# Performance work log

Measured on AMD Instinct MI355X. Metric: run time of the kernel, lower is better.

The kernel has to match this reference:

```python
import jax, jax.numpy as jnp
import numpy as np

N = 8192
H = 512
TAU = 0.8
LAM = 0.5
EPS = 1e-8


def setup_inputs() -> dict:
    key = jax.random.key(0)
    k1, k2, k3, k4, k5 = jax.random.split(key, 5)
    xavier_std = 1.414 * np.sqrt(2.0 / (H + H))  # xavier_normal_ with gain=1.414
    return {
        "z_mp": jax.random.normal(k1, (N, H), dtype=jnp.float32),
        "z_sc": jax.random.normal(k2, (N, H), dtype=jnp.float32),
        "pos": jax.random.randint(k3, (N, N), 0, 2, dtype=jnp.int32),
        "W1": (jax.random.normal(k4, (H, H), dtype=jnp.float32) * xavier_std),
        "b1": jnp.zeros((H,), dtype=jnp.float32),
        "W2": (jax.random.normal(k5, (H, H), dtype=jnp.float32) * xavier_std),
        "b2": jnp.zeros((H,), dtype=jnp.float32),
    }


def _proj(z, W1, b1, W2, b2):
    # nn.Linear applies x @ W.T + b
    h = jax.nn.elu(z @ W1.T + b1)
    return h @ W2.T + b2


def _sim(z1, z2, tau):
    # exp(cosine_similarity / tau), computed as in the original:
    # dot(z1, z2.T) / (|z1| |z2|.T) / tau
    n1 = jnp.linalg.norm(z1, axis=-1, keepdims=True)  # [N,1]
    n2 = jnp.linalg.norm(z2, axis=-1, keepdims=True)  # [N,1]
    dot = z1 @ z2.T                                   # [N,N]
    return jnp.exp(dot / (n1 * n2.T) / tau)


def reference(z_mp, z_sc, pos, W1, b1, W2, b2):
    pos_f = pos.astype(jnp.float32)
    zp_mp = _proj(z_mp, W1, b1, W2, b2)
    zp_sc = _proj(z_sc, W1, b1, W2, b2)

    m_mp2sc = _sim(zp_mp, zp_sc, TAU)   # [N,N]
    m_sc2mp = m_mp2sc.T                 # [N,N]

    # row-normalize, masked log-mean (mp -> sc)
    s_mp = m_mp2sc / (jnp.sum(m_mp2sc, axis=1, keepdims=True) + EPS)
    lori_mp = -jnp.mean(jnp.log(jnp.sum(s_mp * pos_f, axis=-1)))

    # row-normalize, masked log-mean (sc -> mp)
    s_sc = m_sc2mp / (jnp.sum(m_sc2mp, axis=1, keepdims=True) + EPS)
    lori_sc = -jnp.mean(jnp.log(jnp.sum(s_sc * pos_f, axis=-1)))

    return LAM * lori_mp + (1.0 - LAM) * lori_sc
```

## Files before the change

### kernel.cpp

```cpp
#include <hip/hip_runtime.h>
#include <stdint.h>


#define NN 8192
#define HH 512
#define TAUF 0.8f
#define EPSF 1e-8f
#define NW (NN / 32)

typedef __attribute__((ext_vector_type(8))) short short8;
typedef __attribute__((ext_vector_type(4))) float f32x4;
typedef __attribute__((ext_vector_type(4))) int i32x4;
typedef __attribute__((ext_vector_type(4))) unsigned short u16x4;
typedef unsigned short u16;
typedef unsigned int u32;

typedef __attribute__((address_space(1))) void GV;
typedef __attribute__((address_space(3))) void LV;

__device__ __forceinline__ void g2l16(const void* g, void* l) {
  __builtin_amdgcn_global_load_lds((const GV*)g, (LV*)l, 16, 0, 0);
}

__device__ __forceinline__ u16 f2bf(float x) {
  u32 u = __builtin_bit_cast(u32, x);
  u = (u + 0x7fffu + ((u >> 16) & 1u)) >> 16;
  return (u16)u;
}

__device__ __forceinline__ void cast8(const float* __restrict__ in, u16* __restrict__ out, int i) {
  f32x4 a = *(const f32x4*)(in + i);
  f32x4 b = *(const f32x4*)(in + i + 4);
  u16 o[8];
  o[0] = f2bf(a.x); o[1] = f2bf(a.y); o[2] = f2bf(a.z); o[3] = f2bf(a.w);
  o[4] = f2bf(b.x); o[5] = f2bf(b.y); o[6] = f2bf(b.z); o[7] = f2bf(b.w);
  i32x4 v;
  v.x = (int)(o[0] | ((u32)o[1] << 16)); v.y = (int)(o[2] | ((u32)o[3] << 16));
  v.z = (int)(o[4] | ((u32)o[5] << 16)); v.w = (int)(o[6] | ((u32)o[7] << 16));
  *(i32x4*)(out + i) = v;
}

__global__ __launch_bounds__(256)
void prep_kernel(const int* __restrict__ pos, u32* __restrict__ P,
                 const float* __restrict__ z_mp, u16* __restrict__ zbA,
                 const float* __restrict__ z_sc, u16* __restrict__ zbB,
                 const float* __restrict__ W1, u16* __restrict__ W1b,
                 const float* __restrict__ W2, u16* __restrict__ W2b) {
  int b = blockIdx.x, tid = threadIdx.x;
  if (b < 8192) {
    int gid = b * 256 + tid;
    const int* src = pos + (size_t)gid * 32;
    u32 w = 0;
#pragma unroll
    for (int c = 0; c < 8; ++c) {
      i32x4 p = *(const i32x4*)(src + c * 4);
      w |= ((u32)p.x & 1u) << (c * 4);
      w |= ((u32)p.y & 1u) << (c * 4 + 1);
      w |= ((u32)p.z & 1u) << (c * 4 + 2);
      w |= ((u32)p.w & 1u) << (c * 4 + 3);
    }
    P[gid] = w;
  } else if (b < 10240) {
    cast8(z_mp, zbA, ((b - 8192) * 256 + tid) * 8);
  } else if (b < 12288) {
    cast8(z_sc, zbB, ((b - 10240) * 256 + tid) * 8);
  } else if (b < 12416) {
    cast8(W1, W1b, ((b - 12288) * 256 + tid) * 8);
  } else {
    cast8(W2, W2b, ((b - 12416) * 256 + tid) * 8);
  }
}

template <int EPI>
__global__ __launch_bounds__(256)
void gemm_proj(const u16* __restrict__ A1, const u16* __restrict__ A2,
               const u16* __restrict__ W, const float* __restrict__ bias,
               void* __restrict__ out1, void* __restrict__ out2) {
  __shared__ __align__(16) u16 As[128 * 32];
  __shared__ __align__(16) u16 Bs[128 * 32];
  const int tid = threadIdx.x;
  const int lane = tid & 63, w = tid >> 6;
  const int lo = lane & 15, quad = lane >> 4;
  const int wy = w >> 1, wx = w & 1;
  const u16* A; char* Out; int m0;
  if (blockIdx.y < 64) { A = A1; Out = (char*)out1; m0 = blockIdx.y * 128; }
  else                 { A = A2; Out = (char*)out2; m0 = (blockIdx.y - 64) * 128; }
  const int n0 = blockIdx.x * 128;
  const int srow = w * 16 + (lane >> 2);
  const int skel = (lane & 3) * 8;
  char* AsB = (char*)As; char* BsB = (char*)Bs;
  f32x4 acc[4][4] = {};

  for (int k0 = 0; k0 < HH; k0 += 32) {
    const u16* ga = A + (size_t)(m0 + srow) * HH + k0 + skel;
    const u16* gb = W + (size_t)(n0 + srow) * HH + k0 + skel;
    g2l16(ga, AsB + w * 1024);
    g2l16(ga + (size_t)64 * HH, AsB + w * 1024 + 4096);
    g2l16(gb, BsB + w * 1024);
    g2l16(gb + (size_t)64 * HH, BsB + w * 1024 + 4096);
    asm volatile("s_waitcnt vmcnt(0)" ::: "memory");
    __syncthreads();
    short8 aF[4], bF[4];
#pragma unroll
    for (int mi = 0; mi < 4; ++mi)
      aF[mi] = *(const short8*)(AsB + (wy * 64 + mi * 16 + lo) * 64 + quad * 16);
#pragma unroll
    for (int ni = 0; ni < 4; ++ni)
      bF[ni] = *(const short8*)(BsB + (wx * 64 + ni * 16 + lo) * 64 + quad * 16);
#pragma unroll
    for (int mi = 0; mi < 4; ++mi)
#pragma unroll
      for (int ni = 0; ni < 4; ++ni)
        acc[mi][ni] = __builtin_amdgcn_mfma_f32_16x16x32_bf16(aF[mi], bF[ni], acc[mi][ni], 0, 0, 0);
    __syncthreads();
  }
#pragma unroll
  for (int mi = 0; mi < 4; ++mi) {
    int rl = wy * 64 + mi * 16 + quad * 4;
#pragma unroll
    for (int ni = 0; ni < 4; ++ni) {
      int cl = wx * 64 + ni * 16 + lo;
      float bv = bias[n0 + cl];
#pragma unroll
      for (int r = 0; r < 4; ++r) {
        float v = acc[mi][ni][r] + bv;
        size_t idx = (size_t)(m0 + rl + r) * HH + (n0 + cl);
        if (EPI == 0) {
          if (v < 0.f) v = __expf(v) - 1.f;
          ((u16*)Out)[idx] = f2bf(v);
        } else {
          ((float*)Out)[idx] = v;
        }
      }
    }
  }
}

__global__ void norm_kernel(const float* __restrict__ zpA, u16* __restrict__ znA,
                            const float* __restrict__ zpB, u16* __restrict__ znB) {
  const int row = blockIdx.x & (NN - 1);
  const bool isA = blockIdx.x < NN;
  const float* src = (isA ? zpA : zpB) + (size_t)row * HH;
  u16* dst = (isA ? znA : znB) + (size_t)row * HH;
  const float scale = isA ? (1.0f / TAUF) : 1.0f;
  const int t = threadIdx.x;
  f32x4 v = *(const f32x4*)(src + t * 4);
  float ss = v.x * v.x + v.y * v.y + v.z * v.z + v.w * v.w;
#pragma unroll
  for (int d = 1; d < 64; d <<= 1) ss += __shfl_xor(ss, d, 64);
  __shared__ float red[2];
  if ((t & 63) == 0) red[t >> 6] = ss;
  __syncthreads();
  float inv = scale * rsqrtf(red[0] + red[1]);
  u16x4 o;
  o[0] = f2bf(v.x * inv); o[1] = f2bf(v.y * inv);
  o[2] = f2bf(v.z * inv); o[3] = f2bf(v.w * inv);
  *(u16x4*)(dst + t * 4) = o;
}

__global__ __launch_bounds__(256)
void sim_kernel(const u16* __restrict__ Az, const u16* __restrict__ Bz,
                const u32* __restrict__ Pbits,
                float* __restrict__ rowpart, float* __restrict__ posrowpart,
                float* __restrict__ colpart, float* __restrict__ poscolpart) {
  __shared__ __align__(16) u16 As[128 * 64];
  __shared__ __align__(16) u16 Bs[128 * 64];
  __shared__ u32 PBi[128 * 4];
  __shared__ u32 PBj[128 * 4];
  const int tid = threadIdx.x;
  const int lane = tid & 63, w = tid >> 6;
  const int lo = lane & 15, quad = lane >> 4;
  const int wy = w >> 1, wx = w & 1;

  const int bid = blockIdx.x + (int)gridDim.x * blockIdx.y;
  const int xcd = bid & 7, s = bid >> 3;
  const int by = xcd * 8 + (s >> 6);
  const int bx = s & 63;
  const int i0 = by * 128, j0 = bx * 128;

  const int il = tid >> 1, w2 = (tid & 1) * 2;
  const u32* PiSrc = Pbits + (size_t)(i0 + il) * NW + (j0 >> 5) + w2;
  const u32* PjSrc = Pbits + (size_t)(j0 + il) * NW + (i0 >> 5) + w2;
  u32 pa0 = PiSrc[0], pa1 = PiSrc[1], pb0 = PjSrc[0], pb1 = PjSrc[1];

  const int srow = lane >> 3;
  const int skel = (lane & 7) * 8;
  char* AsB = (char*)As; char* BsB = (char*)Bs;
  f32x4 acc[4][4] = {};

  for (int k0 = 0; k0 < HH; k0 += 64) {
    const u16* ga = Az + (size_t)(i0 + w * 32 + srow) * HH + k0 + skel;
    const u16* gb = Bz + (size_t)(j0 + w * 32 + srow) * HH + k0 + skel;
#pragma unroll
    for (int t = 0; t < 4; ++t) {
      g2l16(ga + (size_t)(t * 8) * HH, AsB + w * 4096 + t * 1024);
      g2l16(gb + (size_t)(t * 8) * HH, BsB + w * 4096 + t * 1024);
    }
    asm volatile("s_waitcnt vmcnt(0)" ::: "memory");
    __syncthreads();
    short8 aF[4][2], bF[4][2];
#pragma unroll
    for (int mi = 0; mi < 4; ++mi)
#pragma unroll
      for (int ks = 0; ks < 2; ++ks)
        aF[mi][ks] = *(const short8*)(AsB + (wy * 64 + mi * 16 + lo) * 128 + ks * 64 + quad * 16);
#pragma unroll
    for (int ni = 0; ni < 4; ++ni)
#pragma unroll
      for (int ks = 0; ks < 2; ++ks)
        bF[ni][ks] = *(const short8*)(BsB + (wx * 64 + ni * 16 + lo) * 128 + ks * 64 + quad * 16);
#pragma unroll
    for (int ks = 0; ks < 2; ++ks)
#pragma unroll
      for (int mi = 0; mi < 4; ++mi)
#pragma unroll
        for (int ni = 0; ni < 4; ++ni)
          acc[mi][ni] = __builtin_amdgcn_mfma_f32_16x16x32_bf16(aF[mi][ks], bF[ni][ks], acc[mi][ni], 0, 0, 0);
    __syncthreads();
  }

  PBi[il * 4 + w2] = pa0; PBi[il * 4 + w2 + 1] = pa1;
  PBj[il * 4 + w2] = pb0; PBj[il * 4 + w2 + 1] = pb1;

#pragma unroll
  for (int mi = 0; mi < 4; ++mi)
#pragma unroll
    for (int ni = 0; ni < 4; ++ni)
#pragma unroll
      for (int r = 0; r < 4; ++r)
        acc[mi][ni][r] = __expf(acc[mi][ni][r]);

  __syncthreads();

  const int rowb = wy * 64 + quad * 4;
  const int colb = wx * 64 + lo;

#pragma unroll
  for (int mi = 0; mi < 4; ++mi) {
    int rl = rowb + mi * 16;
    float rs[4], pr[4];
#pragma unroll
    for (int r = 0; r < 4; ++r) {
      u32 W0 = PBi[(rl + r) * 4 + wx * 2];
      u32 W1 = PBi[(rl + r) * 4 + wx * 2 + 1];
      float e0 = acc[mi][0][r], e1 = acc[mi][1][r];
      float e2 = acc[mi][2][r], e3 = acc[mi][3][r];
      rs[r] = (e0 + e1) + (e2 + e3);
      pr[r] = (((W0 >> lo) & 1u) ? e0 : 0.f) + (((W0 >> (16 + lo)) & 1u) ? e1 : 0.f) +
              (((W1 >> lo) & 1u) ? e2 : 0.f) + (((W1 >> (16 + lo)) & 1u) ? e3 : 0.f);
    }
#pragma unroll
    for (int d = 1; d < 16; d <<= 1) {
#pragma unroll
      for (int r = 0; r < 4; ++r) {
        rs[r] += __shfl_xor(rs[r], d, 64);
        pr[r] += __shfl_xor(pr[r], d, 64);
      }
    }
    if (lo == 0) {
      float* rp = rowpart + (size_t)(bx * 2 + wx) * NN;
      float* pp = posrowpart + (size_t)(bx * 2 + wx) * NN;
#pragma unroll
      for (int r = 0; r < 4; ++r) {
        rp[i0 + rl + r] = rs[r];
        pp[i0 + rl + r] = pr[r];
      }
    }
  }

#pragma unroll
  for (int ni = 0; ni < 4; ++ni) {
    int cl = colb + ni * 16;
    u32 W0 = PBj[cl * 4 + wy * 2];
    u32 W1 = PBj[cl * 4 + wy * 2 + 1];
    float cs = 0.f, pc = 0.f;
#pragma unroll
    for (int mi = 0; mi < 4; ++mi) {
      u32 W = (mi < 2) ? W0 : W1;
      int sh = (mi & 1) * 16 + quad * 4;
#pragma unroll
      for (int r = 0; r < 4; ++r) {
        float e = acc[mi][ni][r];
        cs += e;
        pc += ((W >> (sh + r)) & 1u) ? e : 0.f;
      }
    }
    cs += __shfl_xor(cs, 16, 64); cs += __shfl_xor(cs, 32, 64);
    pc += __shfl_xor(pc, 16, 64); pc += __shfl_xor(pc, 32, 64);
    if (quad == 0) {
      colpart[(size_t)(by * 2 + wy) * NN + j0 + cl] = cs;
      poscolpart[(size_t)(by * 2 + wy) * NN + j0 + cl] = pc;
    }
  }
}

__global__ __launch_bounds__(256)
void reduce1_kernel(const float* __restrict__ rowpart, const float* __restrict__ posrowpart,
                    const float* __restrict__ colpart, const float* __restrict__ poscolpart,
                    float* __restrict__ red) {
  int t = threadIdx.x;
  int i = blockIdx.x * 128 + (t >> 1);
  int half = t & 1;
  float rs = 0.f, pr = 0.f, cs = 0.f, pc = 0.f;
  for (int s = half * 64; s < half * 64 + 64; ++s) {
    rs += rowpart[(size_t)s * NN + i];
    pr += posrowpart[(size_t)s * NN + i];
    cs += colpart[(size_t)s * NN + i];
    pc += poscolpart[(size_t)s * NN + i];
  }
  rs += __shfl_xor(rs, 1, 64); pr += __shfl_xor(pr, 1, 64);
  cs += __shfl_xor(cs, 1, 64); pc += __shfl_xor(pc, 1, 64);
  float term = (half == 0) ? (__logf(pr / (rs + EPSF)) + __logf(pc / (cs + EPSF))) : 0.f;
#pragma unroll
  for (int d = 2; d < 64; d <<= 1) term += __shfl_xor(term, d, 64);
  __shared__ float rsh[4];
  if ((t & 63) == 0) rsh[t >> 6] = term;
  __syncthreads();
  if (t == 0) red[blockIdx.x] = rsh[0] + rsh[1] + rsh[2] + rsh[3];
}

__global__ void reduce2_kernel(const float* __restrict__ red, float* __restrict__ out) {
  float s = red[threadIdx.x];
#pragma unroll
  for (int d = 1; d < 64; d <<= 1) s += __shfl_xor(s, d, 64);
  if (threadIdx.x == 0) out[0] = -0.5f * s / (float)NN;
}

extern "C" void kernel_launch(void* const* d_in, const int* in_sizes, int n_in,
                              void* d_out, int out_size, void* d_ws, size_t ws_size,
                              hipStream_t stream) {
  const float* z_mp = (const float*)d_in[0];
  const float* z_sc = (const float*)d_in[1];
  const int* pos = (const int*)d_in[2];
  const float* W1 = (const float*)d_in[3];
  const float* b1 = (const float*)d_in[4];
  const float* W2 = (const float*)d_in[5];
  const float* b2 = (const float*)d_in[6];
  float* out = (float*)d_out;

  char* ws = (char*)d_ws;
  u32* Pbits = (u32*)(ws);
  u16* zbA = (u16*)(ws + 8388608);
  u16* zbB = (u16*)(ws + 16777216);
  u16* W1b = (u16*)(ws + 25165824);
  u16* W2b = (u16*)(ws + 25690112);
  u16* hA  = (u16*)(ws + 26214400);
  u16* hB  = (u16*)(ws + 34603008);
  float* zpA = (float*)(ws + 42991616);
  float* zpB = (float*)(ws + 59768832);
  u16* znA = zbA;
  u16* znB = zbB;
  float* rowpart    = (float*)(ws + 26214400);
  float* posrowpart = (float*)(ws + 30408704);
  float* colpart    = (float*)(ws + 34603008);
  float* poscolpart = (float*)(ws + 38797312);
  float* red64 = (float*)(ws + 76546048);

  prep_kernel<<<12544, 256, 0, stream>>>(pos, Pbits, z_mp, zbA, z_sc, zbB, W1, W1b, W2, W2b);

  dim3 gp(4, 128);
  gemm_proj<0><<<gp, 256, 0, stream>>>(zbA, zbB, W1b, b1, hA, hB);
  gemm_proj<1><<<gp, 256, 0, stream>>>(hA, hB, W2b, b2, zpA, zpB);

  norm_kernel<<<2 * NN, 128, 0, stream>>>(zpA, znA, zpB, znB);

  dim3 gs(64, 64);
  sim_kernel<<<gs, 256, 0, stream>>>(znA, znB, Pbits, rowpart, posrowpart, colpart, poscolpart);
  reduce1_kernel<<<64, 256, 0, stream>>>(rowpart, posrowpart, colpart, poscolpart, red64);
  reduce2_kernel<<<1, 64, 0, stream>>>(red64, out);
}
```

Baseline: 584.6 us.

## Quantize normalized embeddings to FP8 and use scaled f8f6f4 MFMA in similarity GEMM

The norm kernel now writes the unit-normalized projections as FP8 E4M3 bytes instead of bf16, and the similarity kernel consumes them with the 16x16x128 scaled f8f6f4 MFMA. K-tiles grow to 128 bytes per row, and the LDS layout uses an XOR swizzle to avoid bank conflicts. The goal is to halve the operand bandwidth and raise matrix throughput in the N×N GEMM. The cost is reduced precision on the cosine dot products, which are then exponentiated, so the loss may drift.

```diff
diff --git a/kernel.cpp b/kernel.cpp
--- a/kernel.cpp
+++ b/kernel.cpp
@@ -11,9 +11,11 @@
 typedef __attribute__((ext_vector_type(8))) short short8;
 typedef __attribute__((ext_vector_type(4))) float f32x4;
 typedef __attribute__((ext_vector_type(4))) int i32x4;
+typedef __attribute__((ext_vector_type(8))) int i32x8;
 typedef __attribute__((ext_vector_type(4))) unsigned short u16x4;
 typedef unsigned short u16;
 typedef unsigned int u32;
+typedef uint8_t u8;
 
 typedef __attribute__((address_space(1))) void GV;
 typedef __attribute__((address_space(3))) void LV;
@@ -26,6 +28,22 @@
   u32 u = __builtin_bit_cast(u32, x);
   u = (u + 0x7fffu + ((u >> 16) & 1u)) >> 16;
   return (u16)u;
+}
+
+__device__ __forceinline__ u32 f2fp8(float x) {
+  u32 u = __builtin_bit_cast(u32, x);
+  u32 s = (u >> 31) << 7;
+  float a = fabsf(x);
+  if (a >= 0.015625f) {
+    u32 b = __builtin_bit_cast(u32, a);
+    b += 0x7FFFFu + ((b >> 20) & 1u);
+    u32 e = (b >> 23) - 127u + 7u;
+    u32 m = (b >> 20) & 7u;
+    return s | (e << 3) | m;
+  } else {
+    int m = (int)rintf(a * 512.0f);
+    return s | (u32)m;
+  }
 }
 
 __device__ __forceinline__ void cast8(const float* __restrict__ in, u16* __restrict__ out, int i) {
@@ -136,12 +154,12 @@
   }
 }
 
-__global__ void norm_kernel(const float* __restrict__ zpA, u16* __restrict__ znA,
-                            const float* __restrict__ zpB, u16* __restrict__ znB) {
+__global__ void norm_kernel(const float* __restrict__ zpA, u8* __restrict__ znA,
+                            const float* __restrict__ zpB, u8* __restrict__ znB) {
   const int row = blockIdx.x & (NN - 1);
   const bool isA = blockIdx.x < NN;
   const float* src = (isA ? zpA : zpB) + (size_t)row * HH;
-  u16* dst = (isA ? znA : znB) + (size_t)row * HH;
+  u8* dst = (isA ? znA : znB) + (size_t)row * HH;
   const float scale = isA ? (1.0f / TAUF) : 1.0f;
   const int t = threadIdx.x;
   f32x4 v = *(const f32x4*)(src + t * 4);
@@ -152,19 +170,18 @@
   if ((t & 63) == 0) red[t >> 6] = ss;
   __syncthreads();
   float inv = scale * rsqrtf(red[0] + red[1]);
-  u16x4 o;
-  o[0] = f2bf(v.x * inv); o[1] = f2bf(v.y * inv);
-  o[2] = f2bf(v.z * inv); o[3] = f2bf(v.w * inv);
-  *(u16x4*)(dst + t * 4) = o;
+  u32 o = f2fp8(v.x * inv) | (f2fp8(v.y * inv) << 8) |
+          (f2fp8(v.z * inv) << 16) | (f2fp8(v.w * inv) << 24);
+  *(u32*)(dst + t * 4) = o;
 }
 
 __global__ __launch_bounds__(256)
-void sim_kernel(const u16* __restrict__ Az, const u16* __restrict__ Bz,
+void sim_kernel(const u8* __restrict__ Az, const u8* __restrict__ Bz,
                 const u32* __restrict__ Pbits,
                 float* __restrict__ rowpart, float* __restrict__ posrowpart,
                 float* __restrict__ colpart, float* __restrict__ poscolpart) {
-  __shared__ __align__(16) u16 As[128 * 64];
-  __shared__ __align__(16) u16 Bs[128 * 64];
+  __shared__ __align__(16) u8 As[128 * 128];
+  __shared__ __align__(16) u8 Bs[128 * 128];
   __shared__ u32 PBi[128 * 4];
   __shared__ u32 PBj[128 * 4];
   const int tid = threadIdx.x;
@@ -184,13 +201,13 @@
   u32 pa0 = PiSrc[0], pa1 = PiSrc[1], pb0 = PjSrc[0], pb1 = PjSrc[1];
 
   const int srow = lane >> 3;
-  const int skel = (lane & 7) * 8;
+  const int schunk = ((lane & 7) ^ srow) * 16;
   char* AsB = (char*)As; char* BsB = (char*)Bs;
   f32x4 acc[4][4] = {};
 
-  for (int k0 = 0; k0 < HH; k0 += 64) {
-    const u16* ga = Az + (size_t)(i0 + w * 32 + srow) * HH + k0 + skel;
-    const u16* gb = Bz + (size_t)(j0 + w * 32 + srow) * HH + k0 + skel;
+  for (int k0 = 0; k0 < HH; k0 += 128) {
+    const u8* ga = Az + (size_t)(i0 + w * 32 + srow) * HH + k0 + schunk;
+    const u8* gb = Bz + (size_t)(j0 + w * 32 + srow) * HH + k0 + schunk;
 #pragma unroll
     for (int t = 0; t < 4; ++t) {
       g2l16(ga + (size_t)(t * 8) * HH, AsB + w * 4096 + t * 1024);
@@ -198,24 +215,29 @@
     }
     asm volatile("s_waitcnt vmcnt(0)" ::: "memory");
     __syncthreads();
-    short8 aF[4][2], bF[4][2];
+    i32x8 aF[4], bF[4];
+#pragma unroll
+    for (int mi = 0; mi < 4; ++mi) {
+      int ar = wy * 64 + mi * 16 + lo;
+      int sw = ar & 7;
+      i32x4 p0 = *(const i32x4*)(AsB + ar * 128 + ((2 * quad) ^ sw) * 16);
+      i32x4 p1 = *(const i32x4*)(AsB + ar * 128 + ((2 * quad + 1) ^ sw) * 16);
+      aF[mi] = __builtin_shufflevector(p0, p1, 0, 1, 2, 3, 4, 5, 6, 7);
+    }
+#pragma unroll
+    for (int ni = 0; ni < 4; ++ni) {
+      int br = wx * 64 + ni * 16 + lo;
+      int sw = br & 7;
+      i32x4 p0 = *(const i32x4*)(BsB + br * 128 + ((2 * quad) ^ sw) * 16);
+      i32x4 p1 = *(const i32x4*)(BsB + br * 128 + ((2 * quad + 1) ^ sw) * 16);
+      bF[ni] = __builtin_shufflevector(p0, p1, 0, 1, 2, 3, 4, 5, 6, 7);
+    }
 #pragma unroll
     for (int mi = 0; mi < 4; ++mi)
 #pragma unroll
-      for (int ks = 0; ks < 2; ++ks)
-        aF[mi][ks] = *(const short8*)(AsB + (wy * 64 + mi * 16 + lo) * 128 + ks * 64 + quad * 16);
-#pragma unroll
-    for (int ni = 0; ni < 4; ++ni)
-#pragma unroll
-      for (int ks = 0; ks < 2; ++ks)
-        bF[ni][ks] = *(const short8*)(BsB + (wx * 64 + ni * 16 + lo) * 128 + ks * 64 + quad * 16);
-#pragma unroll
-    for (int ks = 0; ks < 2; ++ks)
-#pragma unroll
-      for (int mi = 0; mi < 4; ++mi)
-#pragma unroll
-        for (int ni = 0; ni < 4; ++ni)
-          acc[mi][ni] = __builtin_amdgcn_mfma_f32_16x16x32_bf16(aF[mi][ks], bF[ni][ks], acc[mi][ni], 0, 0, 0);
+      for (int ni = 0; ni < 4; ++ni)
+        acc[mi][ni] = __builtin_amdgcn_mfma_scale_f32_16x16x128_f8f6f4(
+            aF[mi], bF[ni], acc[mi][ni], 0, 0, 0, 127, 0, 127);
     __syncthreads();
   }
 
@@ -348,8 +370,8 @@
   u16* hB  = (u16*)(ws + 34603008);
   float* zpA = (float*)(ws + 42991616);
   float* zpB = (float*)(ws + 59768832);
-  u16* znA = zbA;
-  u16* znB = zbB;
+  u8* znA = (u8*)zbA;
+  u8* znB = (u8*)zbB;
   float* rowpart    = (float*)(ws + 26214400);
   float* posrowpart = (float*)(ws + 30408704);
   float* colpart    = (float*)(ws + 34603008);
```

New measurement: 534.3 us. 8.6% less time.
